# Performance work log

Measured on AMD Instinct MI355X. Metric: run time of the kernel, lower is better.

Reference implementation:

```python
import jax, jax.numpy as jnp
import numpy as np

ALPHA = 0.2   # curvature threshold (init arg alpha)
BETA = 0.5    # ODE step weight (init arg beta)
BIG = 1e9     # sentinel used by torch.where(den < alpha, 1e9, den)


def setup_inputs() -> dict:
    key = jax.random.key(0)
    ks = jax.random.split(key, 6)
    B, N, D = 8, 128, 256
    return {
        "node_inputs": jax.random.normal(ks[0], (B * N, D), jnp.float32),
        "edges_input": jax.random.normal(ks[1], (B * N * N, D), jnp.float32),
        "W_n2e": jax.random.normal(ks[2], (2 * D, D), jnp.float32) * 0.05,
        "b_n2e": jnp.zeros((D,), jnp.float32),
        "W_e2v1": jax.random.normal(ks[3], (D, D // 2), jnp.float32) * 0.05,
        "b_e2v1": jnp.zeros((D // 2,), jnp.float32),
        "W_e2v2": jax.random.normal(ks[4], (D // 2, 1), jnp.float32) * 0.05,
        "b_e2v2": jnp.zeros((1,), jnp.float32),
        "num_atoms": N,
    }


def calc_k(e):
    # e: [B, N, N] nonnegative edge values (relu output).
    # Faithful vectorization of the torch nonzero/scatter/max code:
    # for each masked edge (i, j), denominator = max over row (i resp. j) where
    # entries < alpha OR at columns {i, j} are replaced by 1e9 (the scattered
    # zeros are < alpha so they also become 1e9). We get the exact row max
    # excluding columns {i, j} from the per-row top-3, then max with BIG.
    B, N, _ = e.shape
    mask = (e >= ALPHA) & (e < 1.0)
    r = jnp.where(e < ALPHA, BIG, e)                 # [B, N, N]
    vals, idx = jax.lax.top_k(r, 3)                   # [B, N, 3]
    ar = jnp.arange(N)
    # den_i: uses row i's top-k; exclude entries at columns i (dim 1) and j (dim 2)
    excl_i = (idx[:, :, None, :] == ar[None, :, None, None]) | \
             (idx[:, :, None, :] == ar[None, None, :, None])   # [B, N, N, 3]
    den_i = jnp.maximum(
        jnp.max(jnp.where(excl_i, -jnp.inf, vals[:, :, None, :]), axis=-1), BIG)
    # den_j: uses row j's top-k; same column exclusions
    excl_j = (idx[:, None, :, :] == ar[None, :, None, None]) | \
             (idx[:, None, :, :] == ar[None, None, :, None])
    den_j = jnp.maximum(
        jnp.max(jnp.where(excl_j, -jnp.inf, vals[:, None, :, :]), axis=-1), BIG)
    num = jnp.where(mask, e, 1.0)  # safe value where unmasked (sqrt-grad safety)
    s = jnp.sqrt(num / den_i) + jnp.sqrt(num / den_j)
    cur = jnp.where(mask, s, 0.0)
    return 2.0 - cur.reshape(-1)                      # [B*N*N]


def reference(node_inputs, edges_input, W_n2e, b_n2e, W_e2v1, b_e2v1,
              W_e2v2, b_e2v2, num_atoms):
    N = num_atoms
    D = node_inputs.shape[1]
    x = node_inputs.reshape(-1, N, D)                 # [B, N, D]
    # rel_send/rel_rec one-hot matmuls == direct gathers (row-major edge order)
    send = jnp.arange(N * N) // N
    rec = jnp.arange(N * N) % N
    edges = jnp.concatenate([x[:, send, :], x[:, rec, :]], axis=-1)  # [B, N*N, 2D]
    ez = jax.nn.gelu(edges @ W_n2e + b_n2e, approximate=False)       # [B, N*N, D]
    # dropout p=0.0 -> identity
    h = jax.nn.relu(ez @ W_e2v1 + b_e2v1)             # [B, N*N, D/2]
    e2v = jax.nn.relu((h @ W_e2v2 + b_e2v2)[..., 0])  # [B, N*N]
    ez_flat = ez.reshape(-1, D)                       # [B*N*N, D]
    k = calc_k(e2v.reshape(-1, N, N))[:, None]        # [B*N*N, 1], broadcast over D
    sig = jax.nn.sigmoid(ez_flat)
    grad1 = (k - jnp.exp(sig)) * edges_input
    return ez_flat + BETA * grad1, e2v
```

## Files before the change

### kernel.cpp

```cpp
#include <hip/hip_runtime.h>
#include <cmath>

typedef __attribute__((ext_vector_type(8))) short bf16x8;
typedef __attribute__((ext_vector_type(4))) float f32x4;
typedef unsigned short u16;
typedef unsigned int u32;

#define OUT1OFF 33554432

__device__ __forceinline__ u16 f2bf(float f) {
  union { float f; u32 u; } v; v.f = f;
  u32 r = v.u + 0x7fffu + ((v.u >> 16) & 1u);
  return (u16)(r >> 16);
}

__device__ __forceinline__ float frcp(float x) {
  float r;
  asm("v_rcp_f32 %0, %1" : "=v"(r) : "v"(x));
  return r;
}

__device__ __forceinline__ u32 cvt_pk_bf16(float lo, float hi) {
  u32 r;
  asm("v_cvt_pk_bf16_f32 %0, %1, %2" : "=v"(r) : "v"(lo), "v"(hi));
  return r;
}

__device__ __forceinline__ float gelu_t(float x) {
  const float x2 = x * x;
  const float z = 1.5957691216057308f * x * fmaf(0.044715f, x2, 1.0f);
  return x * frcp(1.0f + __expf(-z));
}

__global__ __launch_bounds__(256) void k1_prep(
    const float* __restrict__ x, const float* __restrict__ Wn2e,
    const float* __restrict__ bn2e, const float* __restrict__ W1,
    float* __restrict__ Uw, float* __restrict__ Yw, u16* __restrict__ W1F)
{
  __shared__ float xl[4][256];
  const int t = threadIdx.x;
  const int blk = blockIdx.x;
  const int r0 = blk * 4;
  {
    const int rr = t >> 6, c4 = (t & 63) * 4;
    *(float4*)&xl[rr][c4] = *(const float4*)&x[(r0 + rr) * 256 + c4];
  }
  __syncthreads();
  const int c = t;
  float u0=0.f,u1=0.f,u2=0.f,u3=0.f,y0=0.f,y1=0.f,y2=0.f,y3=0.f;
  #pragma unroll 4
  for (int k = 0; k < 256; ++k) {
    const float wt = Wn2e[k * 256 + c];
    const float wb = Wn2e[(k + 256) * 256 + c];
    const float a0 = xl[0][k], a1 = xl[1][k], a2 = xl[2][k], a3 = xl[3][k];
    u0 = fmaf(a0, wt, u0); u1 = fmaf(a1, wt, u1);
    u2 = fmaf(a2, wt, u2); u3 = fmaf(a3, wt, u3);
    y0 = fmaf(a0, wb, y0); y1 = fmaf(a1, wb, y1);
    y2 = fmaf(a2, wb, y2); y3 = fmaf(a3, wb, y3);
  }
  const float bb = bn2e[c];
  Uw[(r0+0)*256+c]=u0; Uw[(r0+1)*256+c]=u1; Uw[(r0+2)*256+c]=u2; Uw[(r0+3)*256+c]=u3;
  Yw[(r0+0)*256+c]=y0+bb; Yw[(r0+1)*256+c]=y1+bb; Yw[(r0+2)*256+c]=y2+bb; Yw[(r0+3)*256+c]=y3+bb;
  if (blk < 64) {
    #pragma unroll
    for (int q = 0; q < 2; ++q) {
      const int e = (blk * 256 + t) * 2 + q;
      const int d = e & 7, lf = (e >> 3) & 63, ks = (e >> 9) & 7, nt = (e >> 12) & 7;
      const int n = nt * 16 + (lf & 15);
      const int kg = ks * 32 + ((lf >> 4) & 3) * 8 + d;
      W1F[e] = f2bf(W1[kg * 128 + n]);
    }
  }
}

__global__ __launch_bounds__(256, 4) void k2_fused(
    const float* __restrict__ Uw, const float* __restrict__ Yw,
    const u16* __restrict__ W1F, const float* __restrict__ b1,
    const float* __restrict__ W2, const float* __restrict__ b2p,
    const float* __restrict__ E, float* __restrict__ out)
{
  __shared__ u16 ezLds[64 * 256];
  const int t = threadIdx.x;
  const int blk = blockIdx.x;
  const int pair = blk >> 1;
  const int j0 = (blk & 1) * 64;
  const int b = pair >> 7;
  const int rw = t >> 6;
  const int l = t & 63;
  const int c4 = l * 4;

  const float4 uv = *(const float4*)&Uw[pair * 256 + c4];

  const int rowBase = j0 + rw * 16;
  const int g0 = pair * 128 + rowBase;
  const float* __restrict__ Erow = &E[g0 * 256 + c4];
  const float* __restrict__ Yrow = &Yw[(b * 128 + rowBase) * 256 + c4];
  float* __restrict__ Orow = &out[g0 * 256 + c4];

#define LE(r)  (*(const f32x4*)&Erow[(r) * 256])
#define LY(r)  (*(const float4*)&Yrow[(r) * 256])
#define ROW(it, ev, yv) {                                                   \
    const float ez0 = gelu_t(uv.x + (yv).x);                                \
    const float ez1 = gelu_t(uv.y + (yv).y);                                \
    const float ez2 = gelu_t(uv.z + (yv).z);                                \
    const float ez3 = gelu_t(uv.w + (yv).w);                                \
    uint2 pk;                                                               \
    pk.x = cvt_pk_bf16(ez0, ez1);                                           \
    pk.y = cvt_pk_bf16(ez2, ez3);                                           \
    const int jl = rw * 16 + (it);                                          \
    const int idx = (jl * 256 + c4) ^ ((jl & 7) << 3);                      \
    *(uint2*)&ezLds[idx] = pk;                                              \
    f32x4 o;                                                                \
    o.x = ez0 + (1.f - 0.5f * __expf(frcp(1.f + __expf(-ez0)))) * (ev).x;   \
    o.y = ez1 + (1.f - 0.5f * __expf(frcp(1.f + __expf(-ez1)))) * (ev).y;   \
    o.z = ez2 + (1.f - 0.5f * __expf(frcp(1.f + __expf(-ez2)))) * (ev).z;   \
    o.w = ez3 + (1.f - 0.5f * __expf(frcp(1.f + __expf(-ez3)))) * (ev).w;   \
    __builtin_nontemporal_store(o, (f32x4*)&Orow[(it) * 256]);              \
  }

  f32x4 e0 = LE(0), e1 = LE(1), e2 = LE(2), e3 = LE(3);
  #pragma unroll
  for (int g = 0; g < 4; ++g) {
    f32x4 n0, n1, n2, n3;
    if (g < 3) { n0 = LE(g*4+4); n1 = LE(g*4+5); n2 = LE(g*4+6); n3 = LE(g*4+7); }
    const float4 y0 = LY(g*4+0), y1 = LY(g*4+1), y2 = LY(g*4+2), y3 = LY(g*4+3);
    ROW(g*4+0, e0, y0);
    ROW(g*4+1, e1, y1);
    ROW(g*4+2, e2, y2);
    ROW(g*4+3, e3, y3);
    if (g < 3) { e0 = n0; e1 = n1; e2 = n2; e3 = n3; }
  }
#undef LE
#undef LY
#undef ROW

  const int l15 = l & 15, lh = l >> 4;
  f32x4 acc[8];
  #pragma unroll
  for (int nt = 0; nt < 8; ++nt) acc[nt] = (f32x4){0.f, 0.f, 0.f, 0.f};
  #pragma unroll
  for (int ks = 0; ks < 8; ++ks) {
    const int k = ks * 32 + lh * 8;
    const int aidx = ((rw * 16 + l15) * 256 + k) ^ ((l15 & 7) << 3);
    const bf16x8 a = *(const bf16x8*)&ezLds[aidx];
    #pragma unroll
    for (int nt = 0; nt < 8; ++nt) {
      const bf16x8 bv = *(const bf16x8*)&W1F[(((nt << 3) | ks) * 64 + l) * 8];
      acc[nt] = __builtin_amdgcn_mfma_f32_16x16x32_bf16(a, bv, acc[nt], 0, 0, 0);
    }
  }
  float ps0=0.f, ps1=0.f, ps2=0.f, ps3=0.f;
  #pragma unroll
  for (int nt = 0; nt < 8; ++nt) {
    const int col = nt * 16 + l15;
    const float bv = b1[col], wvv = W2[col];
    ps0 += fmaxf(acc[nt][0] + bv, 0.f) * wvv;
    ps1 += fmaxf(acc[nt][1] + bv, 0.f) * wvv;
    ps2 += fmaxf(acc[nt][2] + bv, 0.f) * wvv;
    ps3 += fmaxf(acc[nt][3] + bv, 0.f) * wvv;
  }
  #pragma unroll
  for (int m = 1; m < 16; m <<= 1) {
    ps0 += __shfl_xor(ps0, m, 64);
    ps1 += __shfl_xor(ps1, m, 64);
    ps2 += __shfl_xor(ps2, m, 64);
    ps3 += __shfl_xor(ps3, m, 64);
  }
  const float b2 = b2p[0];
  const float e2v0 = fmaxf(ps0 + b2, 0.f);
  const float e2v1 = fmaxf(ps1 + b2, 0.f);
  const float e2v2 = fmaxf(ps2 + b2, 0.f);
  const float e2v3 = fmaxf(ps3 + b2, 0.f);
  const int srcLane = ((l15 >> 2) << 4) | l15;
  const float s0 = __shfl(e2v0, srcLane, 64);
  const float s1 = __shfl(e2v1, srcLane, 64);
  const float s2 = __shfl(e2v2, srcLane, 64);
  const float s3 = __shfl(e2v3, srcLane, 64);
  const float t01 = (l15 & 1) ? s1 : s0;
  const float t23 = (l15 & 1) ? s3 : s2;
  const float s = (l15 & 2) ? t23 : t01;
  if (l < 16) out[OUT1OFF + g0 + l] = s;
}

extern "C" void kernel_launch(void* const* d_in, const int* in_sizes, int n_in,
                              void* d_out, int out_size, void* d_ws, size_t ws_size,
                              hipStream_t stream) {
  const float* x    = (const float*)d_in[0];
  const float* E    = (const float*)d_in[1];
  const float* Wn2e = (const float*)d_in[2];
  const float* bn2e = (const float*)d_in[3];
  const float* W1   = (const float*)d_in[4];
  const float* b1   = (const float*)d_in[5];
  const float* W2   = (const float*)d_in[6];
  const float* b2   = (const float*)d_in[7];
  float* out = (float*)d_out;

  float* Uw = (float*)d_ws;
  float* Yw = Uw + 262144;
  u16*  W1F = (u16*)(Yw + 262144);

  hipLaunchKernelGGL(k1_prep, dim3(256), dim3(256), 0, stream,
                     x, Wn2e, bn2e, W1, Uw, Yw, W1F);
  hipLaunchKernelGGL(k2_fused, dim3(2048), dim3(256), 0, stream,
                     Uw, Yw, W1F, b1, W2, b2, E, out);
}
```

Before: 88.86 us.

## Interleave rows across waves and issue all edge loads upfront

```diff
diff --git a/kernel.cpp b/kernel.cpp
--- a/kernel.cpp
+++ b/kernel.cpp
@@ -89,17 +89,34 @@
   const int l = t & 63;
   const int c4 = l * 4;
 
-  const float4 uv = *(const float4*)&Uw[pair * 256 + c4];
-
-  const int rowBase = j0 + rw * 16;
-  const int g0 = pair * 128 + rowBase;
-  const float* __restrict__ Erow = &E[g0 * 256 + c4];
-  const float* __restrict__ Yrow = &Yw[(b * 128 + rowBase) * 256 + c4];
-  float* __restrict__ Orow = &out[g0 * 256 + c4];
-
-#define LE(r)  (*(const f32x4*)&Erow[(r) * 256])
-#define LY(r)  (*(const float4*)&Yrow[(r) * 256])
-#define ROW(it, ev, yv) {                                                   \
+  const f32x4 uv = *(const f32x4*)&Uw[pair * 256 + c4];
+
+  const int eBase = (pair * 128 + j0) * 256 + c4;
+  const int yBase = (b * 128 + j0) * 256 + c4;
+
+  f32x4 v0  = *(const f32x4*)&E[eBase + (0*4+rw)*256];
+  f32x4 v1  = *(const f32x4*)&E[eBase + (1*4+rw)*256];
+  f32x4 v2  = *(const f32x4*)&E[eBase + (2*4+rw)*256];
+  f32x4 v3  = *(const f32x4*)&E[eBase + (3*4+rw)*256];
+  f32x4 v4  = *(const f32x4*)&E[eBase + (4*4+rw)*256];
+  f32x4 v5  = *(const f32x4*)&E[eBase + (5*4+rw)*256];
+  f32x4 v6  = *(const f32x4*)&E[eBase + (6*4+rw)*256];
+  f32x4 v7  = *(const f32x4*)&E[eBase + (7*4+rw)*256];
+  f32x4 v8  = *(const f32x4*)&E[eBase + (8*4+rw)*256];
+  f32x4 v9  = *(const f32x4*)&E[eBase + (9*4+rw)*256];
+  f32x4 v10 = *(const f32x4*)&E[eBase + (10*4+rw)*256];
+  f32x4 v11 = *(const f32x4*)&E[eBase + (11*4+rw)*256];
+  f32x4 v12 = *(const f32x4*)&E[eBase + (12*4+rw)*256];
+  f32x4 v13 = *(const f32x4*)&E[eBase + (13*4+rw)*256];
+  f32x4 v14 = *(const f32x4*)&E[eBase + (14*4+rw)*256];
+  f32x4 v15 = *(const f32x4*)&E[eBase + (15*4+rw)*256];
+  asm volatile("" : "+v"(v0),"+v"(v1),"+v"(v2),"+v"(v3),
+                    "+v"(v4),"+v"(v5),"+v"(v6),"+v"(v7),
+                    "+v"(v8),"+v"(v9),"+v"(v10),"+v"(v11),
+                    "+v"(v12),"+v"(v13),"+v"(v14),"+v"(v15));
+
+#define ROWP(it, ev, yv) {                                                  \
+    const int jj = (it) * 4 + rw;                                           \
     const float ez0 = gelu_t(uv.x + (yv).x);                                \
     const float ez1 = gelu_t(uv.y + (yv).y);                                \
     const float ez2 = gelu_t(uv.z + (yv).z);                                \
@@ -107,41 +124,43 @@
     uint2 pk;                                                               \
     pk.x = cvt_pk_bf16(ez0, ez1);                                           \
     pk.y = cvt_pk_bf16(ez2, ez3);                                           \
-    const int jl = rw * 16 + (it);                                          \
-    const int idx = (jl * 256 + c4) ^ ((jl & 7) << 3);                      \
+    const int idx = (jj * 256 + c4) ^ ((jj & 7) << 3);                      \
     *(uint2*)&ezLds[idx] = pk;                                              \
     f32x4 o;                                                                \
     o.x = ez0 + (1.f - 0.5f * __expf(frcp(1.f + __expf(-ez0)))) * (ev).x;   \
     o.y = ez1 + (1.f - 0.5f * __expf(frcp(1.f + __expf(-ez1)))) * (ev).y;   \
     o.z = ez2 + (1.f - 0.5f * __expf(frcp(1.f + __expf(-ez2)))) * (ev).z;   \
     o.w = ez3 + (1.f - 0.5f * __expf(frcp(1.f + __expf(-ez3)))) * (ev).w;   \
-    __builtin_nontemporal_store(o, (f32x4*)&Orow[(it) * 256]);              \
-  }
-
-  f32x4 e0 = LE(0), e1 = LE(1), e2 = LE(2), e3 = LE(3);
-  #pragma unroll
-  for (int g = 0; g < 4; ++g) {
-    f32x4 n0, n1, n2, n3;
-    if (g < 3) { n0 = LE(g*4+4); n1 = LE(g*4+5); n2 = LE(g*4+6); n3 = LE(g*4+7); }
-    const float4 y0 = LY(g*4+0), y1 = LY(g*4+1), y2 = LY(g*4+2), y3 = LY(g*4+3);
-    ROW(g*4+0, e0, y0);
-    ROW(g*4+1, e1, y1);
-    ROW(g*4+2, e2, y2);
-    ROW(g*4+3, e3, y3);
-    if (g < 3) { e0 = n0; e1 = n1; e2 = n2; e3 = n3; }
-  }
-#undef LE
-#undef LY
-#undef ROW
+    __builtin_nontemporal_store(o, (f32x4*)&out[eBase + jj * 256]);         \
+  }
+#define YGROUP(g, ya0, ya1, ya2, ya3) \
+    f32x4 ya0 = *(const f32x4*)&Yw[yBase + ((g*4+0)*4+rw)*256];             \
+    f32x4 ya1 = *(const f32x4*)&Yw[yBase + ((g*4+1)*4+rw)*256];             \
+    f32x4 ya2 = *(const f32x4*)&Yw[yBase + ((g*4+2)*4+rw)*256];             \
+    f32x4 ya3 = *(const f32x4*)&Yw[yBase + ((g*4+3)*4+rw)*256];             \
+    asm volatile("" : "+v"(ya0), "+v"(ya1), "+v"(ya2), "+v"(ya3));
+
+  { YGROUP(0, ya0, ya1, ya2, ya3)
+    ROWP(0, v0, ya0); ROWP(1, v1, ya1); ROWP(2, v2, ya2); ROWP(3, v3, ya3); }
+  { YGROUP(1, yb0, yb1, yb2, yb3)
+    ROWP(4, v4, yb0); ROWP(5, v5, yb1); ROWP(6, v6, yb2); ROWP(7, v7, yb3); }
+  { YGROUP(2, yc0, yc1, yc2, yc3)
+    ROWP(8, v8, yc0); ROWP(9, v9, yc1); ROWP(10, v10, yc2); ROWP(11, v11, yc3); }
+  { YGROUP(3, yd0, yd1, yd2, yd3)
+    ROWP(12, v12, yd0); ROWP(13, v13, yd1); ROWP(14, v14, yd2); ROWP(15, v15, yd3); }
+#undef ROWP
+#undef YGROUP
+  __syncthreads();
 
   const int l15 = l & 15, lh = l >> 4;
+  const int m0 = rw * 16;
   f32x4 acc[8];
   #pragma unroll
   for (int nt = 0; nt < 8; ++nt) acc[nt] = (f32x4){0.f, 0.f, 0.f, 0.f};
   #pragma unroll
   for (int ks = 0; ks < 8; ++ks) {
     const int k = ks * 32 + lh * 8;
-    const int aidx = ((rw * 16 + l15) * 256 + k) ^ ((l15 & 7) << 3);
+    const int aidx = ((m0 + l15) * 256 + k) ^ ((l15 & 7) << 3);
     const bf16x8 a = *(const bf16x8*)&ezLds[aidx];
     #pragma unroll
     for (int nt = 0; nt < 8; ++nt) {
@@ -179,7 +198,7 @@
   const float t01 = (l15 & 1) ? s1 : s0;
   const float t23 = (l15 & 1) ? s3 : s2;
   const float s = (l15 & 2) ? t23 : t01;
-  if (l < 16) out[OUT1OFF + g0 + l] = s;
+  if (l < 16) out[OUT1OFF + pair * 128 + j0 + m0 + l] = s;
 }
 
 extern "C" void kernel_launch(void* const* d_in, const int* in_sizes, int n_in,
```

After: 92.19 us. 1.04x slower.
